# Optimization experiments

Hardware: AMD Instinct MI355X
Metric: run time of the kernel (lower is better)

Reference implementation:

```python
import jax, jax.numpy as jnp
import numpy as np

B = 16384

def _linear_params(key, out_dim, in_dim):
    k1, k2 = jax.random.split(key)
    s = 1.0 / np.sqrt(in_dim)
    W = jax.random.uniform(k1, (out_dim, in_dim), jnp.float32, -s, s)
    b = jax.random.uniform(k2, (out_dim,), jnp.float32, -s, s)
    return W, b

def setup_inputs() -> dict:
    key = jax.random.key(0)
    ks = jax.random.split(key, 6)
    x = jax.random.normal(ks[0], (B, 784), jnp.float32)
    conv_w = jax.random.normal(ks[1], (3, 3), jnp.float32)
    W1, b1 = _linear_params(ks[2], 1024, 26 * 26)
    W2, b2 = _linear_params(ks[3], 512, 1024)
    W3, b3 = _linear_params(ks[4], 256, 512)
    W4, b4 = _linear_params(ks[5], 10, 256)
    return {"x": x, "conv_w": conv_w, "W1": W1, "b1": b1, "W2": W2, "b2": b2,
            "W3": W3, "b3": b3, "W4": W4, "b4": b4}

def reference(x, conv_w, W1, b1, W2, b2, W3, b3, W4, b4):
    b = x.shape[0]
    img = x.reshape(b, 1, 28, 28)                       # NCHW
    kern = conv_w.reshape(1, 1, 3, 3)                   # OIHW; cross-correlation
    y = jax.lax.conv_general_dilated(img, kern, (1, 1), 'VALID')  # [B,1,26,26]
    h = y.reshape(b, 26 * 26)
    h = jax.nn.relu(h @ W1.T + b1)
    h = jax.nn.relu(h @ W2.T + b2)
    h = jax.nn.relu(h @ W3.T + b3)
    return h @ W4.T + b4                                # [B,10] logits
```

## Files before the change

### kernel.cpp

```cpp
#include <hip/hip_runtime.h>
#include <hip/hip_bf16.h>
#include <stdint.h>

#define BDIM 256

typedef __attribute__((ext_vector_type(8))) short short8;
typedef __attribute__((ext_vector_type(4))) float f32x4;

#define AS1 __attribute__((address_space(1)))
#define AS3 __attribute__((address_space(3)))
#define GLL16(g, s) __builtin_amdgcn_global_load_lds((AS1 const void*)(g), (AS3 void*)(s), 16, 0, 0)

__device__ __forceinline__ unsigned short f2bf(float f) {
  union { float f; unsigned u; } v; v.f = f;
  unsigned r = v.u + 0x7fffu + ((v.u >> 16) & 1u);
  return (unsigned short)(r >> 16);
}
__device__ __forceinline__ float bf2f(unsigned short u) {
  union { unsigned u; float f; } v; v.u = ((unsigned)u) << 16;
  return v.f;
}

template <int N> __device__ __forceinline__ void vmwait() {
  static_assert(N == 0 || N == 2 || N == 4 || N == 6 || N == 8, "unsupported vmcnt");
  if constexpr (N == 8)      asm volatile("s_waitcnt vmcnt(8)" ::: "memory");
  else if constexpr (N == 6) asm volatile("s_waitcnt vmcnt(6)" ::: "memory");
  else if constexpr (N == 4) asm volatile("s_waitcnt vmcnt(4)" ::: "memory");
  else if constexpr (N == 2) asm volatile("s_waitcnt vmcnt(2)" ::: "memory");
  else                       asm volatile("s_waitcnt vmcnt(0)" ::: "memory");
  __builtin_amdgcn_sched_barrier(0);
}

__global__ __launch_bounds__(BDIM) void cast_pad_w1(const float* __restrict__ w,
                                                    unsigned short* __restrict__ o) {
  int idx = blockIdx.x * BDIM + threadIdx.x;
  if (idx >= 1024 * 704) return;
  int n = idx / 704, k = idx - n * 704;
  float v = (k < 676) ? w[n * 676 + k] : 0.f;
  o[idx] = f2bf(v);
}

__global__ __launch_bounds__(BDIM) void cast_plain(const float* __restrict__ w,
                                                   unsigned short* __restrict__ o, int count) {
  int idx = blockIdx.x * BDIM + threadIdx.x;
  if (idx < count) o[idx] = f2bf(w[idx]);
}

__global__ __launch_bounds__(BDIM) void conv3x3(const float* __restrict__ x,
                                                const float* __restrict__ cw,
                                                unsigned short* __restrict__ h0) {
  __shared__ float xs[784];
  __shared__ float w[9];
  int m = blockIdx.x;
  const float* xr = x + (size_t)m * 784;
  if (threadIdx.x < 9) w[threadIdx.x] = cw[threadIdx.x];
  for (int i = threadIdx.x; i < 784; i += BDIM) xs[i] = xr[i];
  __syncthreads();
  unsigned short* hr = h0 + (size_t)m * 704;
  for (int p = threadIdx.x; p < 704; p += BDIM) {
    float v = 0.f;
    if (p < 676) {
      int r = p / 26, c = p - r * 26;
      const float* xp = &xs[r * 28 + c];
      v = xp[0]  * w[0] + xp[1]  * w[1] + xp[2]  * w[2]
        + xp[28] * w[3] + xp[29] * w[4] + xp[30] * w[5]
        + xp[56] * w[6] + xp[57] * w[7] + xp[58] * w[8];
    }
    hr[p] = f2bf(v);
  }
}

template <int BM, int BN, int WGM, bool RELU>
__global__ __launch_bounds__(512, 2) void gemm_bt3(const unsigned short* __restrict__ A,
                                                   const unsigned short* __restrict__ Wt,
                                                   const float* __restrict__ bias,
                                                   unsigned short* __restrict__ Cb,
                                                   int M, int N, int K) {
  constexpr int WGN = 8 / WGM;
  constexpr int FM = BM / WGM / 16;
  constexpr int FN = BN / WGN / 16;
  constexpr int RA = BM / 64;
  constexpr int RB = BN / 64;
  constexpr int NPH = (FM == 8) ? 4 : 2;
  constexpr int MPG = FM / NPH;
  __shared__ unsigned short lds[(size_t)(BM + BN) * 128];
  unsigned short* const Asb = lds;
  unsigned short* const Bsb = lds + 2 * BM * 64;

  const int tid = threadIdx.x;
  const int lane = tid & 63;
  const int wid = tid >> 6;

  const int nbm = M / BM, nbc = N / BN;
  int brow, bcol;
  if (nbm * nbc == 256) {
    const int nid = ((int)blockIdx.x % 8) * 32 + ((int)blockIdx.x / 8);
    const int bpr = 32 / nbc;
    brow = ((nid >> 5) * bpr + (nid & 31) / nbc) * BM;
    bcol = (nid % nbc) * BN;
  } else {
    brow = ((int)blockIdx.x % nbm) * BM;
    bcol = ((int)blockIdx.x / nbm) * BN;
  }

  const int srow = tid >> 3;
  const int sslot = (tid & 7) ^ (srow & 7);
  const unsigned short* gA = A + (size_t)(brow + srow) * K + sslot * 8;
  const unsigned short* gB = Wt + (size_t)(bcol + srow) * K + sslot * 8;
  const int sdst = tid * 8;

#define STAGE_A(buf, kt)                                                      \
  do { _Pragma("unroll")                                                      \
    for (int r = 0; r < RA; ++r)                                              \
      GLL16(gA + (size_t)r * 64 * K + (size_t)(kt) * 64,                      \
            Asb + (buf) * BM * 64 + r * 4096 + sdst);                         \
  } while (0)
#define STAGE_BH(buf, kt, hh)                                                 \
  do { _Pragma("unroll")                                                      \
    for (int r = (hh) * (RB / 2); r < ((hh) + 1) * (RB / 2); ++r)             \
      GLL16(gB + (size_t)r * 64 * K + (size_t)(kt) * 64,                      \
            Bsb + (buf) * BN * 64 + r * 4096 + sdst);                         \
  } while (0)

  f32x4 acc[FM][FN] = {};
  const int fr = lane & 15;
  const int h = lane >> 4;
  const int fx = fr & 7;
  const int abase = (wid / WGN) * (FM * 16);
  const int bbase = (wid % WGN) * (FN * 16);

  const int nk = K >> 6;
  STAGE_A(0, 0);
  STAGE_BH(0, 0, 0); STAGE_BH(0, 0, 1);
  STAGE_BH(1, 1, 0); STAGE_BH(1, 1, 1);
  vmwait<RB>();
  __builtin_amdgcn_s_barrier();
  __builtin_amdgcn_sched_barrier(0);

  for (int kt = 0; kt < nk; ++kt) {
    const int cur = kt & 1;
    const unsigned short* As0 = Asb + cur * BM * 64;
    const unsigned short* Bs0 = Bsb + cur * BN * 64;
    short8 bf[FN][2];
#pragma unroll
    for (int ph = 0; ph < NPH; ++ph) {
      if (ph == 0) {
#pragma unroll
        for (int n = 0; n < FN; ++n)
#pragma unroll
          for (int s = 0; s < 2; ++s)
            bf[n][s] = *(const short8*)&Bs0[(bbase + n * 16 + fr) * 64 + ((((s << 2) + h) ^ fx) << 3)];
      }
      short8 af[MPG][2];
#pragma unroll
      for (int mm = 0; mm < MPG; ++mm)
#pragma unroll
        for (int s = 0; s < 2; ++s)
          af[mm][s] = *(const short8*)&As0[(abase + (ph * MPG + mm) * 16 + fr) * 64 + ((((s << 2) + h) ^ fx) << 3)];
      if (ph == 0) { if (kt + 1 < nk) STAGE_A(cur ^ 1, kt + 1); }
      if (NPH == 4) {
        if (ph == 1 && kt + 2 < nk) STAGE_BH(cur, kt + 2, 0);
        if (ph == 2 && kt + 2 < nk) STAGE_BH(cur, kt + 2, 1);
      } else {
        if (ph == 1 && kt + 2 < nk) { STAGE_BH(cur, kt + 2, 0); STAGE_BH(cur, kt + 2, 1); }
      }
      __builtin_amdgcn_sched_barrier(0);
      __builtin_amdgcn_s_barrier();
      __builtin_amdgcn_sched_barrier(0);
      __builtin_amdgcn_s_setprio(1);
#pragma unroll
      for (int s = 0; s < 2; ++s)
#pragma unroll
        for (int mm = 0; mm < MPG; ++mm)
#pragma unroll
          for (int n = 0; n < FN; ++n)
            acc[ph * MPG + mm][n] =
                __builtin_amdgcn_mfma_f32_16x16x32_bf16(af[mm][s], bf[n][s], acc[ph * MPG + mm][n], 0, 0, 0);
      __builtin_amdgcn_s_setprio(0);
      __builtin_amdgcn_sched_barrier(0);
      if (ph == NPH - 1) {
        if (kt + 2 < nk) vmwait<RB>();
        else             vmwait<0>();
      }
      __builtin_amdgcn_s_barrier();
      __builtin_amdgcn_sched_barrier(0);
    }
  }
#undef STAGE_A
#undef STAGE_BH

  unsigned short* const scr = lds;
  const int lrow0 = abase + (h << 2);
  const int lcol0 = bbase + fr;
#pragma unroll
  for (int n = 0; n < FN; ++n) {
    const int col = lcol0 + n * 16;
    const float bv = bias[bcol + col];
#pragma unroll
    for (int m = 0; m < FM; ++m) {
#pragma unroll
      for (int j = 0; j < 4; ++j) {
        const int row = lrow0 + m * 16 + j;
        float v = acc[m][n][j] + bv;
        if (RELU) v = v > 0.f ? v : 0.f;
        scr[(row * BN + col) ^ ((row & 12) << 2)] = f2bf(v);
      }
    }
  }
  __syncthreads();
  constexpr int CPR = BN / 8;
  constexpr int TOT = BM * CPR;
#pragma unroll 2
  for (int i = tid; i < TOT; i += 512) {
    const int row = i / CPR, c = i % CPR;
    const int cs = c ^ ((row & 12) >> 1);
    short8 vv = *(const short8*)&scr[row * BN + cs * 8];
    *(short8*)(Cb + (size_t)(brow + row) * N + bcol + c * 8) = vv;
  }
}

__global__ __launch_bounds__(BDIM) void fc10(const unsigned short* __restrict__ h3,
                                             const float* __restrict__ W4,
                                             const float* __restrict__ b4,
                                             float* __restrict__ out) {
  int lane = threadIdx.x & 63;
  int wid = threadIdx.x >> 6;
  int m = blockIdx.x * 4 + wid;
  const unsigned short* hr = h3 + (size_t)m * 256 + lane * 4;
  uint64_t hv = *(const uint64_t*)hr;
  float e0 = bf2f((unsigned short)hv), e1 = bf2f((unsigned short)(hv >> 16));
  float e2 = bf2f((unsigned short)(hv >> 32)), e3 = bf2f((unsigned short)(hv >> 48));
#pragma unroll
  for (int n = 0; n < 10; ++n) {
    const float4 wv = *(const float4*)(W4 + n * 256 + lane * 4);
    float s = e0 * wv.x + e1 * wv.y + e2 * wv.z + e3 * wv.w;
#pragma unroll
    for (int off = 32; off > 0; off >>= 1) s += __shfl_xor(s, off);
    if (lane == n) out[(size_t)m * 10 + n] = s + b4[n];
  }
}

extern "C" void kernel_launch(void* const* d_in, const int* in_sizes, int n_in,
                              void* d_out, int out_size, void* d_ws, size_t ws_size,
                              hipStream_t stream) {
  const float* x  = (const float*)d_in[0];
  const float* cw = (const float*)d_in[1];
  const float* W1 = (const float*)d_in[2];
  const float* b1 = (const float*)d_in[3];
  const float* W2 = (const float*)d_in[4];
  const float* b2 = (const float*)d_in[5];
  const float* W3 = (const float*)d_in[6];
  const float* b3 = (const float*)d_in[7];
  const float* W4 = (const float*)d_in[8];
  const float* b4 = (const float*)d_in[9];
  float* out = (float*)d_out;

  char* ws = (char*)d_ws;
  unsigned short* h0  = (unsigned short*)(ws);
  unsigned short* h1  = (unsigned short*)(ws + 23068672);
  unsigned short* W1b = (unsigned short*)(ws + 23068672 + 33554432);
  unsigned short* W2b = W1b + 1024 * 704;
  unsigned short* W3b = W2b + 512 * 1024;
  unsigned short* h2  = h0;
  unsigned short* h3  = h1;

  cast_pad_w1<<<2816, BDIM, 0, stream>>>(W1, W1b);
  cast_plain<<<2048, BDIM, 0, stream>>>(W2, W2b, 512 * 1024);
  cast_plain<<<512, BDIM, 0, stream>>>(W3, W3b, 256 * 512);
  conv3x3<<<16384, BDIM, 0, stream>>>(x, cw, h0);

  gemm_bt3<256, 256, 2, true><<<(16384 / 256) * (1024 / 256), 512, 0, stream>>>(
      h0, W1b, b1, h1, 16384, 1024, 704);
  gemm_bt3<256, 128, 4, true><<<(16384 / 256) * (512 / 128), 512, 0, stream>>>(
      h1, W2b, b2, h2, 16384, 512, 1024);
  gemm_bt3<128, 128, 4, true><<<(16384 / 128) * (256 / 128), 512, 0, stream>>>(
      h2, W3b, b3, h3, 16384, 256, 512);
  fc10<<<16384 / 4, BDIM, 0, stream>>>(h3, W4, b4, out);
}
```

Before: 113.2 us.

## Stage GEMM tiles through registers instead of direct global-to-LDS loads

Replaces the direct global_load_lds staging in the three bf16 GEMMs with ordinary vector global loads into registers, which are then written to swizzled LDS after the last MMA phase of each k-step. The pipeline moves from a three-deep split A/B prefetch with explicit vmcnt waits to a register double-buffer that is one tile ahead. This gives the compiler control over when loads are waited on and lets the swizzle be applied on the LDS write. In exchange it uses more VGPRs under a 512x2 launch bound and adds LDS write instructions plus a wait for them inside the loop, so the prefetch distance is shorter.

```diff
diff --git a/kernel.cpp b/kernel.cpp
--- a/kernel.cpp
+++ b/kernel.cpp
@@ -6,10 +6,7 @@
 
 typedef __attribute__((ext_vector_type(8))) short short8;
 typedef __attribute__((ext_vector_type(4))) float f32x4;
-
-#define AS1 __attribute__((address_space(1)))
-#define AS3 __attribute__((address_space(3)))
-#define GLL16(g, s) __builtin_amdgcn_global_load_lds((AS1 const void*)(g), (AS3 void*)(s), 16, 0, 0)
+typedef __attribute__((ext_vector_type(4))) unsigned int u32x4;
 
 __device__ __forceinline__ unsigned short f2bf(float f) {
   union { float f; unsigned u; } v; v.f = f;
@@ -19,16 +16,6 @@
 __device__ __forceinline__ float bf2f(unsigned short u) {
   union { unsigned u; float f; } v; v.u = ((unsigned)u) << 16;
   return v.f;
-}
-
-template <int N> __device__ __forceinline__ void vmwait() {
-  static_assert(N == 0 || N == 2 || N == 4 || N == 6 || N == 8, "unsupported vmcnt");
-  if constexpr (N == 8)      asm volatile("s_waitcnt vmcnt(8)" ::: "memory");
-  else if constexpr (N == 6) asm volatile("s_waitcnt vmcnt(6)" ::: "memory");
-  else if constexpr (N == 4) asm volatile("s_waitcnt vmcnt(4)" ::: "memory");
-  else if constexpr (N == 2) asm volatile("s_waitcnt vmcnt(2)" ::: "memory");
-  else                       asm volatile("s_waitcnt vmcnt(0)" ::: "memory");
-  __builtin_amdgcn_sched_barrier(0);
 }
 
 __global__ __launch_bounds__(BDIM) void cast_pad_w1(const float* __restrict__ w,
@@ -71,7 +58,7 @@
 }
 
 template <int BM, int BN, int WGM, bool RELU>
-__global__ __launch_bounds__(512, 2) void gemm_bt3(const unsigned short* __restrict__ A,
+__global__ __launch_bounds__(512, 2) void gemm_bt4(const unsigned short* __restrict__ A,
                                                    const unsigned short* __restrict__ Wt,
                                                    const float* __restrict__ bias,
                                                    unsigned short* __restrict__ Cb,
@@ -104,22 +91,27 @@
   }
 
   const int srow = tid >> 3;
-  const int sslot = (tid & 7) ^ (srow & 7);
-  const unsigned short* gA = A + (size_t)(brow + srow) * K + sslot * 8;
-  const unsigned short* gB = Wt + (size_t)(bcol + srow) * K + sslot * 8;
-  const int sdst = tid * 8;
-
-#define STAGE_A(buf, kt)                                                      \
+  const unsigned short* gA = A + (size_t)(brow + srow) * K + (tid & 7) * 8;
+  const unsigned short* gB = Wt + (size_t)(bcol + srow) * K + (tid & 7) * 8;
+  const int wslot = ((tid & 7) ^ (srow & 7)) << 3;
+
+  u32x4 avr[RA], bvr[RB];
+
+#define LOADT(kt)                                                             \
   do { _Pragma("unroll")                                                      \
     for (int r = 0; r < RA; ++r)                                              \
-      GLL16(gA + (size_t)r * 64 * K + (size_t)(kt) * 64,                      \
-            Asb + (buf) * BM * 64 + r * 4096 + sdst);                         \
+      avr[r] = *(const u32x4*)(gA + (size_t)r * 64 * K + (size_t)(kt) * 64);  \
+    _Pragma("unroll")                                                         \
+    for (int r = 0; r < RB; ++r)                                              \
+      bvr[r] = *(const u32x4*)(gB + (size_t)r * 64 * K + (size_t)(kt) * 64);  \
   } while (0)
-#define STAGE_BH(buf, kt, hh)                                                 \
+#define WRITET(buf)                                                           \
   do { _Pragma("unroll")                                                      \
-    for (int r = (hh) * (RB / 2); r < ((hh) + 1) * (RB / 2); ++r)             \
-      GLL16(gB + (size_t)r * 64 * K + (size_t)(kt) * 64,                      \
-            Bsb + (buf) * BN * 64 + r * 4096 + sdst);                         \
+    for (int r = 0; r < RA; ++r)                                              \
+      *(u32x4*)(Asb + (buf) * BM * 64 + (r * 64 + srow) * 64 + wslot) = avr[r]; \
+    _Pragma("unroll")                                                         \
+    for (int r = 0; r < RB; ++r)                                              \
+      *(u32x4*)(Bsb + (buf) * BN * 64 + (r * 64 + srow) * 64 + wslot) = bvr[r]; \
   } while (0)
 
   f32x4 acc[FM][FN] = {};
@@ -130,10 +122,12 @@
   const int bbase = (wid % WGN) * (FN * 16);
 
   const int nk = K >> 6;
-  STAGE_A(0, 0);
-  STAGE_BH(0, 0, 0); STAGE_BH(0, 0, 1);
-  STAGE_BH(1, 1, 0); STAGE_BH(1, 1, 1);
-  vmwait<RB>();
+  LOADT(0);
+  WRITET(0);
+  LOADT(1);
+  WRITET(1);
+  asm volatile("s_waitcnt lgkmcnt(0)" ::: "memory");
+  __builtin_amdgcn_sched_barrier(0);
   __builtin_amdgcn_s_barrier();
   __builtin_amdgcn_sched_barrier(0);
 
@@ -157,13 +151,7 @@
 #pragma unroll
         for (int s = 0; s < 2; ++s)
           af[mm][s] = *(const short8*)&As0[(abase + (ph * MPG + mm) * 16 + fr) * 64 + ((((s << 2) + h) ^ fx) << 3)];
-      if (ph == 0) { if (kt + 1 < nk) STAGE_A(cur ^ 1, kt + 1); }
-      if (NPH == 4) {
-        if (ph == 1 && kt + 2 < nk) STAGE_BH(cur, kt + 2, 0);
-        if (ph == 2 && kt + 2 < nk) STAGE_BH(cur, kt + 2, 1);
-      } else {
-        if (ph == 1 && kt + 2 < nk) { STAGE_BH(cur, kt + 2, 0); STAGE_BH(cur, kt + 2, 1); }
-      }
+      if (ph == 0 && kt + 1 < nk) LOADT(kt + 1);
       __builtin_amdgcn_sched_barrier(0);
       __builtin_amdgcn_s_barrier();
       __builtin_amdgcn_sched_barrier(0);
@@ -179,15 +167,18 @@
       __builtin_amdgcn_s_setprio(0);
       __builtin_amdgcn_sched_barrier(0);
       if (ph == NPH - 1) {
-        if (kt + 2 < nk) vmwait<RB>();
-        else             vmwait<0>();
+        if (kt + 1 < nk) {
+          WRITET(cur ^ 1);
+          asm volatile("s_waitcnt lgkmcnt(0)" ::: "memory");
+          __builtin_amdgcn_sched_barrier(0);
+        }
       }
       __builtin_amdgcn_s_barrier();
       __builtin_amdgcn_sched_barrier(0);
     }
   }
-#undef STAGE_A
-#undef STAGE_BH
+#undef LOADT
+#undef WRITET
 
   unsigned short* const scr = lds;
   const int lrow0 = abase + (h << 2);
@@ -269,11 +260,11 @@
   cast_plain<<<512, BDIM, 0, stream>>>(W3, W3b, 256 * 512);
   conv3x3<<<16384, BDIM, 0, stream>>>(x, cw, h0);
 
-  gemm_bt3<256, 256, 2, true><<<(16384 / 256) * (1024 / 256), 512, 0, stream>>>(
+  gemm_bt4<256, 256, 2, true><<<(16384 / 256) * (1024 / 256), 512, 0, stream>>>(
       h0, W1b, b1, h1, 16384, 1024, 704);
-  gemm_bt3<256, 128, 4, true><<<(16384 / 256) * (512 / 128), 512, 0, stream>>>(
+  gemm_bt4<256, 128, 4, true><<<(16384 / 256) * (512 / 128), 512, 0, stream>>>(
       h1, W2b, b2, h2, 16384, 512, 1024);
-  gemm_bt3<128, 128, 4, true><<<(16384 / 128) * (256 / 128), 512, 0, stream>>>(
+  gemm_bt4<128, 128, 4, true><<<(16384 / 128) * (256 / 128), 512, 0, stream>>>(
       h2, W3b, b3, h3, 16384, 256, 512);
   fc10<<<16384 / 4, BDIM, 0, stream>>>(h3, W4, b4, out);
 }
```

Result: slower. 125.2 us (+10.6%).
